# Kernel tuning notes

Measured on AMD Instinct MI355X. Metric: run time of the kernel, lower is better.

Reference implementation:

```python
import jax, jax.numpy as jnp
import numpy as np

N = 100000
E = 1600000
STEPS_IN = 16
IN_DIMS = STEPS_IN + 2  # x concat grid
D = 64  # LATENT_DIMS, mlp_ratio=1 so mid dims == D


def _mlp(x, w1, b1, w2, b2):
    # MLP with mid_dims: Linear -> GELU(exact) -> Linear
    h = jax.nn.gelu(x @ w1 + b1, approximate=False)
    return h @ w2 + b2


def setup_inputs() -> dict:
    key = jax.random.key(0)
    ks = jax.random.split(key, 20)

    def lin(k, fan_in, fan_out):
        bound = 1.0 / np.sqrt(fan_in)
        kw, kb = jax.random.split(k)
        w = jax.random.uniform(kw, (fan_in, fan_out), jnp.float32, -bound, bound)
        b = jax.random.uniform(kb, (fan_out,), jnp.float32, -bound, bound)
        return w, b

    inp = {}
    inp['x'] = jax.random.normal(ks[0], (N, STEPS_IN), jnp.float32)
    inp['grid'] = jax.random.uniform(ks[1], (N, 2), jnp.float32)
    inp['edge_index'] = jax.random.randint(ks[2], (2, E), 0, N, jnp.int64 if jax.config.jax_enable_x64 else jnp.int32)
    inp['edge_features'] = jax.random.normal(ks[3], (E, 5), jnp.float32)

    # project: in_dims -> D (mid D)
    inp['p_w1'], inp['p_b1'] = lin(ks[4], IN_DIMS, D)
    inp['p_w2'], inp['p_b2'] = lin(ks[5], D, D)
    # block W MLP: D -> D (mid D)
    inp['w_w1'], inp['w_b1'] = lin(ks[6], D, D)
    inp['w_w2'], inp['w_b2'] = lin(ks[7], D, D)
    # decode: D -> 1 (mid D)
    inp['d_w1'], inp['d_b1'] = lin(ks[8], D, D)
    inp['d_w2'], inp['d_b2'] = lin(ks[9], D, 1)
    return inp


def reference(x, grid, edge_index, edge_features,
              p_w1, p_b1, p_w2, p_b2,
              w_w1, w_b1, w_w2, w_b2,
              d_w1, d_b1, d_w2, d_b2):
    n = x.shape[0]
    # project node features (x concat grid)
    h = _mlp(jnp.concatenate([x, grid], axis=-1), p_w1, p_b1, p_w2, p_b2)  # [N, D]
    # message passing: message() returns x_j (source features); aggr='add' at target
    src, dst = edge_index[0], edge_index[1]
    msg = h[src]  # [E, D] gather
    aggr = jax.ops.segment_sum(msg, dst, num_segments=n)  # [N, D] scatter-add
    # update (mode 'none'): gelu(W(x) + aggr)
    h = jax.nn.gelu(_mlp(h, w_w1, w_b1, w_w2, w_b2) + aggr, approximate=False)
    # decode to scalar per node
    return _mlp(h, d_w1, d_b1, d_w2, d_b2)  # [N, 1]
```

## Files before the change

### kernel.cpp

```cpp
#include <hip/hip_runtime.h>
#include <math.h>

#define NN 100000
#define NE 1600000
#define D 64
#define INDIM 18
#define CHUNKS 256
#define BN 64
#define NBKT 1563
#define CAP 1536
#define NFRAG 72

typedef __attribute__((ext_vector_type(8))) short s8b;
typedef __attribute__((ext_vector_type(4))) float f32x4;

__device__ __forceinline__ float gelu_exact(float x) {
    return 0.5f * x * (1.0f + erff(x * 0.70710678118654752f));
}

__device__ __forceinline__ void split_bf16(float f, unsigned short& h, unsigned short& l) {
    unsigned int u = __float_as_uint(f);
    unsigned int hb = (u + 0x7FFFu + ((u >> 16) & 1u)) >> 16;
    float hf = __uint_as_float(hb << 16);
    float lo = f - hf;
    unsigned int u2 = __float_as_uint(lo);
    unsigned int lb = (u2 + 0x7FFFu + ((u2 >> 16) & 1u)) >> 16;
    h = (unsigned short)hb; l = (unsigned short)lb;
}

__global__ __launch_bounds__(256) void pack_frags_kernel(
    const float* __restrict__ ww1, const float* __restrict__ ww2,
    const float* __restrict__ dw1, const float* __restrict__ pw1,
    const float* __restrict__ pw2, unsigned short* __restrict__ fragw)
{
    int tid = blockIdx.x * 256 + threadIdx.x;
    if (tid >= NFRAG * 64) return;
    int f = tid >> 6, l = tid & 63;
    unsigned short o[8];
    if (f < 48) {
        int x = f & 1, t = (f >> 1) & 3, s = (f >> 3) & 1, layer = f >> 4;
        const float* W = (layer == 0) ? ww1 : ((layer == 1) ? ww2 : dw1);
        #pragma unroll
        for (int j = 0; j < 8; ++j) {
            int k = s * 32 + (l >> 4) * 8 + j;
            int n = t * 16 + (l & 15);
            unsigned short hh, ll;
            split_bf16(W[k * D + n], hh, ll);
            o[j] = x ? ll : hh;
        }
    } else if (f < 56) {
        int g = f - 48, x = g & 1, t = (g >> 1) & 3;
        #pragma unroll
        for (int j = 0; j < 8; ++j) {
            int k = (l >> 4) * 8 + j;
            int n = t * 16 + (l & 15);
            float v = (k < INDIM) ? pw1[k * D + n] : 0.f;
            unsigned short hh, ll;
            split_bf16(v, hh, ll);
            o[j] = x ? ll : hh;
        }
    } else {
        int g = f - 56, x = g & 1, t = (g >> 1) & 3, s = (g >> 3) & 1;
        #pragma unroll
        for (int j = 0; j < 8; ++j) {
            int k = s * 32 + (l >> 4) * 8 + j;
            int n = t * 16 + (l & 15);
            unsigned short hh, ll;
            split_bf16(pw2[k * D + n], hh, ll);
            o[j] = x ? ll : hh;
        }
    }
    uint4 v;
    v.x = (unsigned)o[0] | ((unsigned)o[1] << 16);
    v.y = (unsigned)o[2] | ((unsigned)o[3] << 16);
    v.z = (unsigned)o[4] | ((unsigned)o[5] << 16);
    v.w = (unsigned)o[6] | ((unsigned)o[7] << 16);
    *(uint4*)&fragw[(size_t)f * 512 + l * 8] = v;
}

__global__ __launch_bounds__(256) void project_mfma(
    const float* __restrict__ x, const float* __restrict__ grid,
    const unsigned short* __restrict__ fragw,
    const float* __restrict__ pb1, const float* __restrict__ pb2,
    float* __restrict__ h)
{
    __shared__ unsigned short midH[64 * 64];
    __shared__ unsigned short midL[64 * 64];
    const int tid = threadIdx.x;
    const int w = tid >> 6, l = tid & 63;
    const int q = l >> 4, c = l & 15;
    const int g0 = blockIdx.x * 64;
    const int rowbase = w * 16;

    union BU { uint4 u; s8b s; };

    const int arow = g0 + rowbase + c;
    const bool ok = arow < NN;
    float fv[8] = {0.f,0.f,0.f,0.f,0.f,0.f,0.f,0.f};
    if (q < 2) {
        if (ok) {
            const float* xp = x + (size_t)arow * 16 + q * 8;
            float4 f0 = *(const float4*)xp;
            float4 f1 = *(const float4*)(xp + 4);
            fv[0]=f0.x; fv[1]=f0.y; fv[2]=f0.z; fv[3]=f0.w;
            fv[4]=f1.x; fv[5]=f1.y; fv[6]=f1.z; fv[7]=f1.w;
        }
    } else if (q == 2) {
        if (ok) {
            float2 g2 = *(const float2*)(grid + (size_t)arow * 2);
            fv[0] = g2.x; fv[1] = g2.y;
        }
    }
    s8b aH[2], aL[2];
    #pragma unroll
    for (int j = 0; j < 8; ++j) {
        unsigned short hh, ll;
        split_bf16(fv[j], hh, ll);
        aH[0][j] = (short)hh; aL[0][j] = (short)ll;
    }

    f32x4 acc[4];
    #pragma unroll
    for (int t = 0; t < 4; ++t) acc[t] = (f32x4){0.f, 0.f, 0.f, 0.f};
    #pragma unroll
    for (int t = 0; t < 4; ++t) {
        BU bh, bl;
        int fb = 48 + t * 2;
        bh.u = *(const uint4*)&fragw[(size_t)fb * 512 + l * 8];
        bl.u = *(const uint4*)&fragw[(size_t)(fb + 1) * 512 + l * 8];
        acc[t] = __builtin_amdgcn_mfma_f32_16x16x32_bf16(aH[0], bh.s, acc[t], 0, 0, 0);
        acc[t] = __builtin_amdgcn_mfma_f32_16x16x32_bf16(aH[0], bl.s, acc[t], 0, 0, 0);
        acc[t] = __builtin_amdgcn_mfma_f32_16x16x32_bf16(aL[0], bh.s, acc[t], 0, 0, 0);
    }

    #pragma unroll
    for (int t = 0; t < 4; ++t) {
        float bias = pb1[t * 16 + c];
        #pragma unroll
        for (int r = 0; r < 4; ++r) {
            int grow = rowbase + q * 4 + r;
            float v = gelu_exact(acc[t][r] + bias);
            unsigned short hh, ll;
            split_bf16(v, hh, ll);
            int byte = ((grow * 128 + (t * 16 + c) * 2)) ^ ((grow & 7) << 4);
            midH[byte >> 1] = hh; midL[byte >> 1] = ll;
        }
    }
    __syncthreads();

    #pragma unroll
    for (int s = 0; s < 2; ++s) {
        int ar = rowbase + c;
        int abyte = (ar * 128 + s * 64 + q * 16) ^ ((ar & 7) << 4);
        aH[s] = *(const s8b*)((const char*)midH + abyte);
        aL[s] = *(const s8b*)((const char*)midL + abyte);
    }
    #pragma unroll
    for (int t = 0; t < 4; ++t) acc[t] = (f32x4){0.f, 0.f, 0.f, 0.f};
    #pragma unroll
    for (int s = 0; s < 2; ++s) {
        #pragma unroll
        for (int t = 0; t < 4; ++t) {
            BU bh, bl;
            int fb = 56 + s * 8 + t * 2;
            bh.u = *(const uint4*)&fragw[(size_t)fb * 512 + l * 8];
            bl.u = *(const uint4*)&fragw[(size_t)(fb + 1) * 512 + l * 8];
            acc[t] = __builtin_amdgcn_mfma_f32_16x16x32_bf16(aH[s], bh.s, acc[t], 0, 0, 0);
            acc[t] = __builtin_amdgcn_mfma_f32_16x16x32_bf16(aH[s], bl.s, acc[t], 0, 0, 0);
            acc[t] = __builtin_amdgcn_mfma_f32_16x16x32_bf16(aL[s], bh.s, acc[t], 0, 0, 0);
        }
    }
    #pragma unroll
    for (int t = 0; t < 4; ++t) {
        float bias = pb2[t * 16 + c];
        #pragma unroll
        for (int r = 0; r < 4; ++r) {
            int row = g0 + rowbase + q * 4 + r;
            if (row < NN) h[(size_t)row * D + t * 16 + c] = acc[t][r] + bias;
        }
    }
}

__global__ __launch_bounds__(256) void project_kernel(
    const float* __restrict__ x, const float* __restrict__ grid,
    const float* __restrict__ w1, const float* __restrict__ b1,
    const float* __restrict__ w2, const float* __restrict__ b2,
    float* __restrict__ h)
{
    int n = blockIdx.x * 256 + threadIdx.x;
    if (n >= NN) return;

    float in[INDIM];
    {
        const float4* xr = (const float4*)(x + (size_t)n * 16);
        float4 a = xr[0], b = xr[1], c = xr[2], d = xr[3];
        in[0]=a.x; in[1]=a.y; in[2]=a.z; in[3]=a.w;
        in[4]=b.x; in[5]=b.y; in[6]=b.z; in[7]=b.w;
        in[8]=c.x; in[9]=c.y; in[10]=c.z; in[11]=c.w;
        in[12]=d.x; in[13]=d.y; in[14]=d.z; in[15]=d.w;
        float2 g = *(const float2*)(grid + (size_t)n * 2);
        in[16]=g.x; in[17]=g.y;
    }

    float mid[D];
    for (int j1 = 0; j1 < D; j1 += 4) {
        float a0 = b1[j1], a1 = b1[j1+1], a2 = b1[j1+2], a3 = b1[j1+3];
        #pragma unroll
        for (int k = 0; k < INDIM; ++k) {
            float t = in[k];
            a0 += t * w1[k*D + j1];
            a1 += t * w1[k*D + j1+1];
            a2 += t * w1[k*D + j1+2];
            a3 += t * w1[k*D + j1+3];
        }
        mid[j1]   = gelu_exact(a0);
        mid[j1+1] = gelu_exact(a1);
        mid[j1+2] = gelu_exact(a2);
        mid[j1+3] = gelu_exact(a3);
    }

    float acc[D];
    #pragma unroll
    for (int j = 0; j < D; ++j) acc[j] = b2[j];
    for (int j1 = 0; j1 < D; j1 += 4) {
        float t0 = mid[j1], t1 = mid[j1+1], t2 = mid[j1+2], t3 = mid[j1+3];
        #pragma unroll
        for (int j = 0; j < D; ++j)
            acc[j] += t0 * w2[j1*D + j]     + t1 * w2[(j1+1)*D + j]
                    + t2 * w2[(j1+2)*D + j] + t3 * w2[(j1+3)*D + j];
    }

    float* hrow = h + (size_t)n * D;
    #pragma unroll
    for (int j = 0; j < D; j += 4) {
        float4 v = { acc[j], acc[j+1], acc[j+2], acc[j+3] };
        *(float4*)(hrow + j) = v;
    }
}

__global__ __launch_bounds__(256) void count_kernel(
    const int* __restrict__ ei, unsigned short* __restrict__ counts)
{
    __shared__ int s_hist[NBKT];
    const int blk = blockIdx.x, tid = threadIdx.x;
    const int* __restrict__ dst = ei + NE;
    for (int i = tid; i < NBKT; i += 256) s_hist[i] = 0;
    __syncthreads();
    for (int e = blk * 256 + tid; e < NE; e += CHUNKS * 256)
        atomicAdd(&s_hist[dst[e] / BN], 1);
    __syncthreads();
    for (int b = tid; b < NBKT; b += 256)
        counts[blk * NBKT + b] = (unsigned short)s_hist[b];
}

__global__ __launch_bounds__(256) void scan_cols_kernel(
    unsigned short* __restrict__ counts, int* __restrict__ btotal)
{
    __shared__ int s[256];
    const int g = blockIdx.x, tid = threadIdx.x;
    int v = counts[tid * NBKT + g];
    s[tid] = v; __syncthreads();
    for (int off = 1; off < 256; off <<= 1) {
        int val = s[tid];
        int add = (tid >= off) ? s[tid - off] : 0;
        __syncthreads();
        s[tid] = val + add;
        __syncthreads();
    }
    counts[tid * NBKT + g] = (unsigned short)(s[tid] - v);
    if (tid == 255) btotal[g] = s[255];
}

__global__ __launch_bounds__(1024) void scan_bsum_kernel(
    const int* __restrict__ btotal, int* __restrict__ offs)
{
    __shared__ int s[1024];
    const int tid = threadIdx.x;
    int b0 = 2 * tid, b1 = 2 * tid + 1;
    int v0 = (b0 < NBKT) ? btotal[b0] : 0;
    int v1 = (b1 < NBKT) ? btotal[b1] : 0;
    int sum = v0 + v1;
    s[tid] = sum; __syncthreads();
    for (int off = 1; off < 1024; off <<= 1) {
        int val = s[tid];
        int add = (tid >= off) ? s[tid - off] : 0;
        __syncthreads();
        s[tid] = val + add;
        __syncthreads();
    }
    int base = s[tid] - sum;
    if (b0 < NBKT) offs[b0] = base;
    if (b1 < NBKT) offs[b1] = base + v0;
    if (tid == 0)  offs[NBKT] = NE;
}

__global__ __launch_bounds__(256) void bin_kernel(
    const int* __restrict__ ei, const unsigned short* __restrict__ counts,
    const int* __restrict__ offs, int* __restrict__ packed)
{
    __shared__ int s_cur[NBKT];
    const int blk = blockIdx.x, tid = threadIdx.x;
    const int* __restrict__ dst = ei + NE;
    for (int b = tid; b < NBKT; b += 256)
        s_cur[b] = offs[b] + (int)counts[blk * NBKT + b];
    __syncthreads();
    for (int e = blk * 256 + tid; e < NE; e += CHUNKS * 256) {
        int d = dst[e];
        int s = ei[e];
        int pos = atomicAdd(&s_cur[d / BN], 1);
        packed[pos] = (s << 6) | (d & (BN - 1));
    }
}

__global__ __launch_bounds__(256) void sortagg_kernel(
    const int* __restrict__ offs, const int* __restrict__ packed,
    const float* __restrict__ h, float* __restrict__ aggr)
{
    __shared__ int s_off[BN + 1];
    __shared__ int s_cur[BN];
    __shared__ int s_src[CAP];
    const int b = blockIdx.x, tid = threadIdx.x;
    const int start = offs[b], end = offs[b + 1];
    const int cnt = end - start;
    const int wid = tid >> 6, lane = tid & 63;
    const int base = b * BN;

    if (cnt <= CAP) {
        if (tid < BN) s_cur[tid] = 0;
        __syncthreads();
        for (int e = start + tid; e < end; e += 256)
            atomicAdd(&s_cur[packed[e] & (BN - 1)], 1);
        __syncthreads();
        if (tid < 64) {
            int v = s_cur[tid];
            int incl = v;
            #pragma unroll
            for (int off = 1; off < 64; off <<= 1) {
                int u = __shfl_up(incl, off, 64);
                if (tid >= off) incl += u;
            }
            s_off[tid] = incl - v;
            if (tid == 63) s_off[64] = cnt;
        }
        __syncthreads();
        if (tid < BN) s_cur[tid] = s_off[tid];
        __syncthreads();
        for (int e = start + tid; e < end; e += 256) {
            int p = packed[e];
            int pos = atomicAdd(&s_cur[p & (BN - 1)], 1);
            s_src[pos] = p >> 6;
        }
        __syncthreads();
        for (int m = wid; m < BN; m += 4) {
            int node = base + m;
            if (node < NN) {
                int s0 = s_off[m], s1 = s_off[m + 1];
                float a0=0,a1=0,a2=0,a3=0,a4=0,a5=0,a6=0,a7=0;
                int e = s0;
                for (; e + 8 <= s1; e += 8) {
                    int i0=s_src[e],  i1=s_src[e+1],i2=s_src[e+2],i3=s_src[e+3];
                    int i4=s_src[e+4],i5=s_src[e+5],i6=s_src[e+6],i7=s_src[e+7];
                    a0 += h[(size_t)i0*D+lane]; a1 += h[(size_t)i1*D+lane];
                    a2 += h[(size_t)i2*D+lane]; a3 += h[(size_t)i3*D+lane];
                    a4 += h[(size_t)i4*D+lane]; a5 += h[(size_t)i5*D+lane];
                    a6 += h[(size_t)i6*D+lane]; a7 += h[(size_t)i7*D+lane];
                }
                for (; e < s1; ++e) a0 += h[(size_t)s_src[e]*D+lane];
                aggr[(size_t)node*D+lane] = ((a0+a1)+(a2+a3))+((a4+a5)+(a6+a7));
            }
        }
    } else {
        for (int m = wid; m < BN; m += 4) {
            int node = base + m;
            if (node < NN) {
                float a = 0.f;
                for (int e = start; e < end; ++e) {
                    int p = packed[e];
                    if ((p & (BN - 1)) == m) a += h[(size_t)(p >> 6) * D + lane];
                }
                aggr[(size_t)node * D + lane] = a;
            }
        }
    }
}

__global__ __launch_bounds__(256) void aggregate_kernel(
    const int* __restrict__ ei, const float* __restrict__ h,
    float* __restrict__ aggr)
{
    int t = blockIdx.x * 256 + threadIdx.x;
    int e = t >> 6;
    int lane = t & 63;
    if (e >= NE) return;
    int src = ei[e];
    int dst = ei[NE + e];
    float v = h[(size_t)src * D + lane];
    atomicAdd(&aggr[(size_t)dst * D + lane], v);
}

__global__ __launch_bounds__(256) void update_decode_mfma(
    const float* __restrict__ h, const float* __restrict__ aggr,
    const unsigned short* __restrict__ fragw,
    const float* __restrict__ wb1, const float* __restrict__ wb2,
    const float* __restrict__ db1, const float* __restrict__ dw2,
    const float* __restrict__ db2, float* __restrict__ out)
{
    __shared__ unsigned short midH[64 * 64];
    __shared__ unsigned short midL[64 * 64];
    const int tid = threadIdx.x;
    const int w = tid >> 6, l = tid & 63;
    const int q = l >> 4, c = l & 15;
    const int g0 = blockIdx.x * 64;
    const int rowbase = w * 16;

    union BU { uint4 u; s8b s; };

    s8b aH[2], aL[2];
    #pragma unroll
    for (int s = 0; s < 2; ++s) {
        const float* hp = h + (size_t)(g0 + rowbase + c) * D + s * 32 + q * 8;
        float4 f0 = *(const float4*)hp;
        float4 f1 = *(const float4*)(hp + 4);
        float fv[8] = {f0.x, f0.y, f0.z, f0.w, f1.x, f1.y, f1.z, f1.w};
        #pragma unroll
        for (int j = 0; j < 8; ++j) {
            unsigned short hh, ll;
            split_bf16(fv[j], hh, ll);
            aH[s][j] = (short)hh; aL[s][j] = (short)ll;
        }
    }

    f32x4 acc[4];
    #pragma unroll
    for (int t = 0; t < 4; ++t) acc[t] = (f32x4){0.f, 0.f, 0.f, 0.f};

    #pragma unroll
    for (int s = 0; s < 2; ++s) {
        #pragma unroll
        for (int t = 0; t < 4; ++t) {
            BU bh, bl;
            int fb = ((0 * 2 + s) * 4 + t) * 2;
            bh.u = *(const uint4*)&fragw[(size_t)fb * 512 + l * 8];
            bl.u = *(const uint4*)&fragw[(size_t)(fb + 1) * 512 + l * 8];
            acc[t] = __builtin_amdgcn_mfma_f32_16x16x32_bf16(aH[s], bh.s, acc[t], 0, 0, 0);
            acc[t] = __builtin_amdgcn_mfma_f32_16x16x32_bf16(aH[s], bl.s, acc[t], 0, 0, 0);
            acc[t] = __builtin_amdgcn_mfma_f32_16x16x32_bf16(aL[s], bh.s, acc[t], 0, 0, 0);
        }
    }

    #pragma unroll
    for (int t = 0; t < 4; ++t) {
        float bias = wb1[t * 16 + c];
        #pragma unroll
        for (int r = 0; r < 4; ++r) {
            int grow = rowbase + q * 4 + r;
            float v = gelu_exact(acc[t][r] + bias);
            unsigned short hh, ll;
            split_bf16(v, hh, ll);
            int byte = ((grow * 128 + (t * 16 + c) * 2)) ^ ((grow & 7) << 4);
            midH[byte >> 1] = hh; midL[byte >> 1] = ll;
        }
    }
    __syncthreads();

    #pragma unroll
    for (int s = 0; s < 2; ++s) {
        int ar = rowbase + c;
        int abyte = (ar * 128 + s * 64 + q * 16) ^ ((ar & 7) << 4);
        aH[s] = *(const s8b*)((const char*)midH + abyte);
        aL[s] = *(const s8b*)((const char*)midL + abyte);
    }
    #pragma unroll
    for (int t = 0; t < 4; ++t) acc[t] = (f32x4){0.f, 0.f, 0.f, 0.f};
    #pragma unroll
    for (int s = 0; s < 2; ++s) {
        #pragma unroll
        for (int t = 0; t < 4; ++t) {
            BU bh, bl;
            int fb = ((1 * 2 + s) * 4 + t) * 2;
            bh.u = *(const uint4*)&fragw[(size_t)fb * 512 + l * 8];
            bl.u = *(const uint4*)&fragw[(size_t)(fb + 1) * 512 + l * 8];
            acc[t] = __builtin_amdgcn_mfma_f32_16x16x32_bf16(aH[s], bh.s, acc[t], 0, 0, 0);
            acc[t] = __builtin_amdgcn_mfma_f32_16x16x32_bf16(aH[s], bl.s, acc[t], 0, 0, 0);
            acc[t] = __builtin_amdgcn_mfma_f32_16x16x32_bf16(aL[s], bh.s, acc[t], 0, 0, 0);
        }
    }
    __syncthreads();

    #pragma unroll
    for (int t = 0; t < 4; ++t) {
        float bias = wb2[t * 16 + c];
        #pragma unroll
        for (int r = 0; r < 4; ++r) {
            int grow = rowbase + q * 4 + r;
            float ag = aggr[(size_t)(g0 + grow) * D + t * 16 + c];
            float v = gelu_exact(acc[t][r] + bias + ag);
            unsigned short hh, ll;
            split_bf16(v, hh, ll);
            int byte = ((grow * 128 + (t * 16 + c) * 2)) ^ ((grow & 7) << 4);
            midH[byte >> 1] = hh; midL[byte >> 1] = ll;
        }
    }
    __syncthreads();

    #pragma unroll
    for (int s = 0; s < 2; ++s) {
        int ar = rowbase + c;
        int abyte = (ar * 128 + s * 64 + q * 16) ^ ((ar & 7) << 4);
        aH[s] = *(const s8b*)((const char*)midH + abyte);
        aL[s] = *(const s8b*)((const char*)midL + abyte);
    }
    #pragma unroll
    for (int t = 0; t < 4; ++t) acc[t] = (f32x4){0.f, 0.f, 0.f, 0.f};
    #pragma unroll
    for (int s = 0; s < 2; ++s) {
        #pragma unroll
        for (int t = 0; t < 4; ++t) {
            BU bh, bl;
            int fb = ((2 * 2 + s) * 4 + t) * 2;
            bh.u = *(const uint4*)&fragw[(size_t)fb * 512 + l * 8];
            bl.u = *(const uint4*)&fragw[(size_t)(fb + 1) * 512 + l * 8];
            acc[t] = __builtin_amdgcn_mfma_f32_16x16x32_bf16(aH[s], bh.s, acc[t], 0, 0, 0);
            acc[t] = __builtin_amdgcn_mfma_f32_16x16x32_bf16(aH[s], bl.s, acc[t], 0, 0, 0);
            acc[t] = __builtin_amdgcn_mfma_f32_16x16x32_bf16(aL[s], bh.s, acc[t], 0, 0, 0);
        }
    }

    float p[4] = {0.f, 0.f, 0.f, 0.f};
    #pragma unroll
    for (int t = 0; t < 4; ++t) {
        float bias = db1[t * 16 + c];
        float wv = dw2[t * 16 + c];
        #pragma unroll
        for (int r = 0; r < 4; ++r)
            p[r] += gelu_exact(acc[t][r] + bias) * wv;
    }
    #pragma unroll
    for (int m = 1; m < 16; m <<= 1) {
        #pragma unroll
        for (int r = 0; r < 4; ++r) p[r] += __shfl_xor(p[r], m, 16);
    }
    if (c == 0) {
        float b2v = db2[0];
        #pragma unroll
        for (int r = 0; r < 4; ++r) {
            int row = g0 + rowbase + q * 4 + r;
            if (row < NN) out[row] = p[r] + b2v;
        }
    }
}

__global__ __launch_bounds__(256) void update_decode_valu(
    const float* __restrict__ h, const float* __restrict__ aggr,
    const float* __restrict__ ww1, const float* __restrict__ wb1,
    const float* __restrict__ ww2, const float* __restrict__ wb2,
    const float* __restrict__ dw1, const float* __restrict__ db1,
    const float* __restrict__ dw2, const float* __restrict__ db2,
    float* __restrict__ out)
{
    int n = blockIdx.x * 256 + threadIdx.x;
    if (n >= NN) return;
    float hrow[D];
    #pragma unroll
    for (int j = 0; j < D; j += 4) {
        float4 v = *(const float4*)(h + (size_t)n * D + j);
        hrow[j] = v.x; hrow[j+1] = v.y; hrow[j+2] = v.z; hrow[j+3] = v.w;
    }
    float mid[D];
    for (int j1 = 0; j1 < D; j1 += 4) {
        float a0 = wb1[j1], a1 = wb1[j1+1], a2 = wb1[j1+2], a3 = wb1[j1+3];
        #pragma unroll
        for (int k = 0; k < D; ++k) {
            float t = hrow[k];
            a0 += t * ww1[k*D + j1];   a1 += t * ww1[k*D + j1+1];
            a2 += t * ww1[k*D + j1+2]; a3 += t * ww1[k*D + j1+3];
        }
        mid[j1]=gelu_exact(a0); mid[j1+1]=gelu_exact(a1);
        mid[j1+2]=gelu_exact(a2); mid[j1+3]=gelu_exact(a3);
    }
    #pragma unroll
    for (int j = 0; j < D; j += 4) {
        float4 v = *(const float4*)(aggr + (size_t)n * D + j);
        hrow[j]=wb2[j]+v.x; hrow[j+1]=wb2[j+1]+v.y;
        hrow[j+2]=wb2[j+2]+v.z; hrow[j+3]=wb2[j+3]+v.w;
    }
    for (int j1 = 0; j1 < D; j1 += 4) {
        float t0=mid[j1], t1=mid[j1+1], t2=mid[j1+2], t3=mid[j1+3];
        #pragma unroll
        for (int j = 0; j < D; ++j)
            hrow[j] += t0*ww2[j1*D+j] + t1*ww2[(j1+1)*D+j]
                     + t2*ww2[(j1+2)*D+j] + t3*ww2[(j1+3)*D+j];
    }
    #pragma unroll
    for (int j = 0; j < D; ++j) hrow[j] = gelu_exact(hrow[j]);
    float o = db2[0];
    for (int j1 = 0; j1 < D; j1 += 4) {
        float a0 = db1[j1], a1 = db1[j1+1], a2 = db1[j1+2], a3 = db1[j1+3];
        #pragma unroll
        for (int k = 0; k < D; ++k) {
            float t = hrow[k];
            a0 += t*dw1[k*D+j1];   a1 += t*dw1[k*D+j1+1];
            a2 += t*dw1[k*D+j1+2]; a3 += t*dw1[k*D+j1+3];
        }
        o += gelu_exact(a0)*dw2[j1] + gelu_exact(a1)*dw2[j1+1]
           + gelu_exact(a2)*dw2[j1+2] + gelu_exact(a3)*dw2[j1+3];
    }
    out[n] = o;
}

extern "C" void kernel_launch(void* const* d_in, const int* in_sizes, int n_in,
                              void* d_out, int out_size, void* d_ws, size_t ws_size,
                              hipStream_t stream) {
    const float* x    = (const float*)d_in[0];
    const float* grid = (const float*)d_in[1];
    const int*   ei   = (const int*)d_in[2];
    const float* p_w1 = (const float*)d_in[4];
    const float* p_b1 = (const float*)d_in[5];
    const float* p_w2 = (const float*)d_in[6];
    const float* p_b2 = (const float*)d_in[7];
    const float* w_w1 = (const float*)d_in[8];
    const float* w_b1 = (const float*)d_in[9];
    const float* w_w2 = (const float*)d_in[10];
    const float* w_b2 = (const float*)d_in[11];
    const float* d_w1 = (const float*)d_in[12];
    const float* d_b1 = (const float*)d_in[13];
    const float* d_w2 = (const float*)d_in[14];
    const float* d_b2 = (const float*)d_in[15];
    float* out = (float*)d_out;

    float* h    = (float*)d_ws;
    float* aggr = h + (size_t)NN * D;
    unsigned short* counts = (unsigned short*)(aggr + (size_t)NN * D);
    int* btotal = (int*)(counts + (size_t)CHUNKS * NBKT);
    int* offs   = btotal + NBKT;
    int* packed = offs + NBKT + 1;
    unsigned short* fragw =
        (unsigned short*)((((uintptr_t)(packed + NE)) + 15) & ~(uintptr_t)15);

    size_t need = ((char*)(fragw + NFRAG * 512)) - (char*)d_ws;

    if (ws_size >= need) {
        pack_frags_kernel<<<(NFRAG * 64 + 255) / 256, 256, 0, stream>>>(
            w_w1, w_w2, d_w1, p_w1, p_w2, fragw);
        project_mfma<<<(NN + 63) / 64, 256, 0, stream>>>(
            x, grid, fragw, p_b1, p_b2, h);
        count_kernel    <<<CHUNKS, 256, 0, stream>>>(ei, counts);
        scan_cols_kernel<<<NBKT,   256, 0, stream>>>(counts, btotal);
        scan_bsum_kernel<<<1,     1024, 0, stream>>>(btotal, offs);
        bin_kernel      <<<CHUNKS, 256, 0, stream>>>(ei, counts, offs, packed);
        sortagg_kernel  <<<NBKT,   256, 0, stream>>>(offs, packed, h, aggr);
        update_decode_mfma<<<(NN + 63) / 64, 256, 0, stream>>>(
            h, aggr, fragw, w_b1, w_b2, d_b1, d_w2, d_b2, out);
    } else {
        project_kernel<<<(NN + 255) / 256, 256, 0, stream>>>(
            x, grid, p_w1, p_b1, p_w2, p_b2, h);
        hipMemsetAsync(aggr, 0, (size_t)NN * D * sizeof(float), stream);
        aggregate_kernel<<<(size_t)NE * 64 / 256, 256, 0, stream>>>(ei, h, aggr);
        update_decode_valu<<<(NN + 255) / 256, 256, 0, stream>>>(
            h, aggr, w_w1, w_b1, w_w2, w_b2, d_w1, d_b1, d_w2, d_b2, out);
    }
}
```

Baseline: 160.1 us.

## Fuse sorted aggregation with update/decode MLP and widen binning chunk count

Merges the per-bucket gather-sum kernel with the update and decode MFMA kernel, keeping the aggregated features in shared memory instead of writing and rereading a global aggr array, and drops one launch. Separately raises CHUNKS from 256 to 1024 so the count and bin kernels run more blocks, with the column scan now handling four counts per thread. The fused kernel uses more shared memory (an extra 64x65 float tile), which can reduce occupancy during the latency-bound gather. The workspace still reserves space sized by CHUNKS, so the size check must accommodate the larger counts array, or the code falls back to the slower path.

```diff
diff --git a/kernel.cpp b/kernel.cpp
--- a/kernel.cpp
+++ b/kernel.cpp
@@ -5,7 +5,7 @@
 #define NE 1600000
 #define D 64
 #define INDIM 18
-#define CHUNKS 256
+#define CHUNKS 1024
 #define BN 64
 #define NBKT 1563
 #define CAP 1536
@@ -250,7 +250,7 @@
         atomicAdd(&s_hist[dst[e] / BN], 1);
     __syncthreads();
     for (int b = tid; b < NBKT; b += 256)
-        counts[blk * NBKT + b] = (unsigned short)s_hist[b];
+        counts[(size_t)blk * NBKT + b] = (unsigned short)s_hist[b];
 }
 
 __global__ __launch_bounds__(256) void scan_cols_kernel(
@@ -258,8 +258,12 @@
 {
     __shared__ int s[256];
     const int g = blockIdx.x, tid = threadIdx.x;
-    int v = counts[tid * NBKT + g];
-    s[tid] = v; __syncthreads();
+    int c[4];
+    #pragma unroll
+    for (int i = 0; i < 4; ++i)
+        c[i] = counts[(size_t)(tid * 4 + i) * NBKT + g];
+    int sum = c[0] + c[1] + c[2] + c[3];
+    s[tid] = sum; __syncthreads();
     for (int off = 1; off < 256; off <<= 1) {
         int val = s[tid];
         int add = (tid >= off) ? s[tid - off] : 0;
@@ -267,7 +271,12 @@
         s[tid] = val + add;
         __syncthreads();
     }
-    counts[tid * NBKT + g] = (unsigned short)(s[tid] - v);
+    int base = s[tid] - sum;
+    #pragma unroll
+    for (int i = 0; i < 4; ++i) {
+        counts[(size_t)(tid * 4 + i) * NBKT + g] = (unsigned short)base;
+        base += c[i];
+    }
     if (tid == 255) btotal[g] = s[255];
 }
 
@@ -302,7 +311,7 @@
     const int blk = blockIdx.x, tid = threadIdx.x;
     const int* __restrict__ dst = ei + NE;
     for (int b = tid; b < NBKT; b += 256)
-        s_cur[b] = offs[b] + (int)counts[blk * NBKT + b];
+        s_cur[b] = offs[b] + (int)counts[(size_t)blk * NBKT + b];
     __syncthreads();
     for (int e = blk * 256 + tid; e < NE; e += CHUNKS * 256) {
         int d = dst[e];
@@ -312,13 +321,19 @@
     }
 }
 
-__global__ __launch_bounds__(256) void sortagg_kernel(
+__global__ __launch_bounds__(256) void sortagg_update_kernel(
     const int* __restrict__ offs, const int* __restrict__ packed,
-    const float* __restrict__ h, float* __restrict__ aggr)
+    const float* __restrict__ h, const unsigned short* __restrict__ fragw,
+    const float* __restrict__ wb1, const float* __restrict__ wb2,
+    const float* __restrict__ db1, const float* __restrict__ dw2,
+    const float* __restrict__ db2, float* __restrict__ out)
 {
     __shared__ int s_off[BN + 1];
     __shared__ int s_cur[BN];
     __shared__ int s_src[CAP];
+    __shared__ float s_aggr[BN][65];
+    __shared__ unsigned short midH[64 * 64];
+    __shared__ unsigned short midL[64 * 64];
     const int b = blockIdx.x, tid = threadIdx.x;
     const int start = offs[b], end = offs[b + 1];
     const int cnt = end - start;
@@ -352,34 +367,169 @@
         }
         __syncthreads();
         for (int m = wid; m < BN; m += 4) {
-            int node = base + m;
-            if (node < NN) {
-                int s0 = s_off[m], s1 = s_off[m + 1];
-                float a0=0,a1=0,a2=0,a3=0,a4=0,a5=0,a6=0,a7=0;
-                int e = s0;
-                for (; e + 8 <= s1; e += 8) {
-                    int i0=s_src[e],  i1=s_src[e+1],i2=s_src[e+2],i3=s_src[e+3];
-                    int i4=s_src[e+4],i5=s_src[e+5],i6=s_src[e+6],i7=s_src[e+7];
-                    a0 += h[(size_t)i0*D+lane]; a1 += h[(size_t)i1*D+lane];
-                    a2 += h[(size_t)i2*D+lane]; a3 += h[(size_t)i3*D+lane];
-                    a4 += h[(size_t)i4*D+lane]; a5 += h[(size_t)i5*D+lane];
-                    a6 += h[(size_t)i6*D+lane]; a7 += h[(size_t)i7*D+lane];
-                }
-                for (; e < s1; ++e) a0 += h[(size_t)s_src[e]*D+lane];
-                aggr[(size_t)node*D+lane] = ((a0+a1)+(a2+a3))+((a4+a5)+(a6+a7));
+            int s0 = s_off[m], s1 = s_off[m + 1];
+            float a0=0,a1=0,a2=0,a3=0,a4=0,a5=0,a6=0,a7=0;
+            int e = s0;
+            for (; e + 8 <= s1; e += 8) {
+                int i0=s_src[e],  i1=s_src[e+1],i2=s_src[e+2],i3=s_src[e+3];
+                int i4=s_src[e+4],i5=s_src[e+5],i6=s_src[e+6],i7=s_src[e+7];
+                a0 += h[(size_t)i0*D+lane]; a1 += h[(size_t)i1*D+lane];
+                a2 += h[(size_t)i2*D+lane]; a3 += h[(size_t)i3*D+lane];
+                a4 += h[(size_t)i4*D+lane]; a5 += h[(size_t)i5*D+lane];
+                a6 += h[(size_t)i6*D+lane]; a7 += h[(size_t)i7*D+lane];
             }
+            for (; e < s1; ++e) a0 += h[(size_t)s_src[e]*D+lane];
+            s_aggr[m][lane] = ((a0+a1)+(a2+a3))+((a4+a5)+(a6+a7));
         }
     } else {
         for (int m = wid; m < BN; m += 4) {
-            int node = base + m;
-            if (node < NN) {
-                float a = 0.f;
-                for (int e = start; e < end; ++e) {
-                    int p = packed[e];
-                    if ((p & (BN - 1)) == m) a += h[(size_t)(p >> 6) * D + lane];
-                }
-                aggr[(size_t)node * D + lane] = a;
+            float a = 0.f;
+            for (int e = start; e < end; ++e) {
+                int p = packed[e];
+                if ((p & (BN - 1)) == m) a += h[(size_t)(p >> 6) * D + lane];
             }
+            s_aggr[m][lane] = a;
+        }
+    }
+    __syncthreads();
+
+    const int w = wid, l = lane;
+    const int q = l >> 4, c = l & 15;
+    const int g0 = base;
+    const int rowbase = w * 16;
+
+    union BU { uint4 u; s8b s; };
+
+    s8b aH[2], aL[2];
+    #pragma unroll
+    for (int s = 0; s < 2; ++s) {
+        const float* hp = h + (size_t)(g0 + rowbase + c) * D + s * 32 + q * 8;
+        float4 f0 = *(const float4*)hp;
+        float4 f1 = *(const float4*)(hp + 4);
+        float fv[8] = {f0.x, f0.y, f0.z, f0.w, f1.x, f1.y, f1.z, f1.w};
+        #pragma unroll
+        for (int j = 0; j < 8; ++j) {
+            unsigned short hh, ll;
+            split_bf16(fv[j], hh, ll);
+            aH[s][j] = (short)hh; aL[s][j] = (short)ll;
+        }
+    }
+
+    f32x4 acc[4];
+    #pragma unroll
+    for (int t = 0; t < 4; ++t) acc[t] = (f32x4){0.f, 0.f, 0.f, 0.f};
+    #pragma unroll
+    for (int s = 0; s < 2; ++s) {
+        #pragma unroll
+        for (int t = 0; t < 4; ++t) {
+            BU bh, bl;
+            int fb = ((0 * 2 + s) * 4 + t) * 2;
+            bh.u = *(const uint4*)&fragw[(size_t)fb * 512 + l * 8];
+            bl.u = *(const uint4*)&fragw[(size_t)(fb + 1) * 512 + l * 8];
+            acc[t] = __builtin_amdgcn_mfma_f32_16x16x32_bf16(aH[s], bh.s, acc[t], 0, 0, 0);
+            acc[t] = __builtin_amdgcn_mfma_f32_16x16x32_bf16(aH[s], bl.s, acc[t], 0, 0, 0);
+            acc[t] = __builtin_amdgcn_mfma_f32_16x16x32_bf16(aL[s], bh.s, acc[t], 0, 0, 0);
+        }
+    }
+
+    #pragma unroll
+    for (int t = 0; t < 4; ++t) {
+        float bias = wb1[t * 16 + c];
+        #pragma unroll
+        for (int r = 0; r < 4; ++r) {
+            int grow = rowbase + q * 4 + r;
+            float v = gelu_exact(acc[t][r] + bias);
+            unsigned short hh, ll;
+            split_bf16(v, hh, ll);
+            int byte = ((grow * 128 + (t * 16 + c) * 2)) ^ ((grow & 7) << 4);
+            midH[byte >> 1] = hh; midL[byte >> 1] = ll;
+        }
+    }
+    __syncthreads();
+
+    #pragma unroll
+    for (int s = 0; s < 2; ++s) {
+        int ar = rowbase + c;
+        int abyte = (ar * 128 + s * 64 + q * 16) ^ ((ar & 7) << 4);
+        aH[s] = *(const s8b*)((const char*)midH + abyte);
+        aL[s] = *(const s8b*)((const char*)midL + abyte);
+    }
+    #pragma unroll
+    for (int t = 0; t < 4; ++t) acc[t] = (f32x4){0.f, 0.f, 0.f, 0.f};
+    #pragma unroll
+    for (int s = 0; s < 2; ++s) {
+        #pragma unroll
+        for (int t = 0; t < 4; ++t) {
+            BU bh, bl;
+            int fb = ((1 * 2 + s) * 4 + t) * 2;
+            bh.u = *(const uint4*)&fragw[(size_t)fb * 512 + l * 8];
+            bl.u = *(const uint4*)&fragw[(size_t)(fb + 1) * 512 + l * 8];
+            acc[t] = __builtin_amdgcn_mfma_f32_16x16x32_bf16(aH[s], bh.s, acc[t], 0, 0, 0);
+            acc[t] = __builtin_amdgcn_mfma_f32_16x16x32_bf16(aH[s], bl.s, acc[t], 0, 0, 0);
+            acc[t] = __builtin_amdgcn_mfma_f32_16x16x32_bf16(aL[s], bh.s, acc[t], 0, 0, 0);
+        }
+    }
+    __syncthreads();
+
+    #pragma unroll
+    for (int t = 0; t < 4; ++t) {
+        float bias = wb2[t * 16 + c];
+        #pragma unroll
+        for (int r = 0; r < 4; ++r) {
+            int grow = rowbase + q * 4 + r;
+            float ag = s_aggr[grow][t * 16 + c];
+            float v = gelu_exact(acc[t][r] + bias + ag);
+            unsigned short hh, ll;
+            split_bf16(v, hh, ll);
+            int byte = ((grow * 128 + (t * 16 + c) * 2)) ^ ((grow & 7) << 4);
+            midH[byte >> 1] = hh; midL[byte >> 1] = ll;
+        }
+    }
+    __syncthreads();
+
+    #pragma unroll
+    for (int s = 0; s < 2; ++s) {
+        int ar = rowbase + c;
+        int abyte = (ar * 128 + s * 64 + q * 16) ^ ((ar & 7) << 4);
+        aH[s] = *(const s8b*)((const char*)midH + abyte);
+        aL[s] = *(const s8b*)((const char*)midL + abyte);
+    }
+    #pragma unroll
+    for (int t = 0; t < 4; ++t) acc[t] = (f32x4){0.f, 0.f, 0.f, 0.f};
+    #pragma unroll
+    for (int s = 0; s < 2; ++s) {
+        #pragma unroll
+        for (int t = 0; t < 4; ++t) {
+            BU bh, bl;
+            int fb = ((2 * 2 + s) * 4 + t) * 2;
+            bh.u = *(const uint4*)&fragw[(size_t)fb * 512 + l * 8];
+            bl.u = *(const uint4*)&fragw[(size_t)(fb + 1) * 512 + l * 8];
+            acc[t] = __builtin_amdgcn_mfma_f32_16x16x32_bf16(aH[s], bh.s, acc[t], 0, 0, 0);
+            acc[t] = __builtin_amdgcn_mfma_f32_16x16x32_bf16(aH[s], bl.s, acc[t], 0, 0, 0);
+            acc[t] = __builtin_amdgcn_mfma_f32_16x16x32_bf16(aL[s], bh.s, acc[t], 0, 0, 0);
+        }
+    }
+
+    float p[4] = {0.f, 0.f, 0.f, 0.f};
+    #pragma unroll
+    for (int t = 0; t < 4; ++t) {
+        float bias = db1[t * 16 + c];
+        float wv = dw2[t * 16 + c];
+        #pragma unroll
+        for (int r = 0; r < 4; ++r)
+            p[r] += gelu_exact(acc[t][r] + bias) * wv;
+    }
+    #pragma unroll
+    for (int m = 1; m < 16; m <<= 1) {
+        #pragma unroll
+        for (int r = 0; r < 4; ++r) p[r] += __shfl_xor(p[r], m, 16);
+    }
+    if (c == 0) {
+        float b2v = db2[0];
+        #pragma unroll
+        for (int r = 0; r < 4; ++r) {
+            int row = g0 + rowbase + q * 4 + r;
+            if (row < NN) out[row] = p[r] + b2v;
         }
     }
 }
@@ -396,158 +546,6 @@
     int dst = ei[NE + e];
     float v = h[(size_t)src * D + lane];
     atomicAdd(&aggr[(size_t)dst * D + lane], v);
-}
-
-__global__ __launch_bounds__(256) void update_decode_mfma(
-    const float* __restrict__ h, const float* __restrict__ aggr,
-    const unsigned short* __restrict__ fragw,
-    const float* __restrict__ wb1, const float* __restrict__ wb2,
-    const float* __restrict__ db1, const float* __restrict__ dw2,
-    const float* __restrict__ db2, float* __restrict__ out)
-{
-    __shared__ unsigned short midH[64 * 64];
-    __shared__ unsigned short midL[64 * 64];
-    const int tid = threadIdx.x;
-    const int w = tid >> 6, l = tid & 63;
-    const int q = l >> 4, c = l & 15;
-    const int g0 = blockIdx.x * 64;
-    const int rowbase = w * 16;
-
-    union BU { uint4 u; s8b s; };
-
-    s8b aH[2], aL[2];
-    #pragma unroll
-    for (int s = 0; s < 2; ++s) {
-        const float* hp = h + (size_t)(g0 + rowbase + c) * D + s * 32 + q * 8;
-        float4 f0 = *(const float4*)hp;
-        float4 f1 = *(const float4*)(hp + 4);
-        float fv[8] = {f0.x, f0.y, f0.z, f0.w, f1.x, f1.y, f1.z, f1.w};
-        #pragma unroll
-        for (int j = 0; j < 8; ++j) {
-            unsigned short hh, ll;
-            split_bf16(fv[j], hh, ll);
-            aH[s][j] = (short)hh; aL[s][j] = (short)ll;
-        }
-    }
-
-    f32x4 acc[4];
-    #pragma unroll
-    for (int t = 0; t < 4; ++t) acc[t] = (f32x4){0.f, 0.f, 0.f, 0.f};
-
-    #pragma unroll
-    for (int s = 0; s < 2; ++s) {
-        #pragma unroll
-        for (int t = 0; t < 4; ++t) {
-            BU bh, bl;
-            int fb = ((0 * 2 + s) * 4 + t) * 2;
-            bh.u = *(const uint4*)&fragw[(size_t)fb * 512 + l * 8];
-            bl.u = *(const uint4*)&fragw[(size_t)(fb + 1) * 512 + l * 8];
-            acc[t] = __builtin_amdgcn_mfma_f32_16x16x32_bf16(aH[s], bh.s, acc[t], 0, 0, 0);
-            acc[t] = __builtin_amdgcn_mfma_f32_16x16x32_bf16(aH[s], bl.s, acc[t], 0, 0, 0);
-            acc[t] = __builtin_amdgcn_mfma_f32_16x16x32_bf16(aL[s], bh.s, acc[t], 0, 0, 0);
-        }
-    }
-
-    #pragma unroll
-    for (int t = 0; t < 4; ++t) {
-        float bias = wb1[t * 16 + c];
-        #pragma unroll
-        for (int r = 0; r < 4; ++r) {
-            int grow = rowbase + q * 4 + r;
-            float v = gelu_exact(acc[t][r] + bias);
-            unsigned short hh, ll;
-            split_bf16(v, hh, ll);
-            int byte = ((grow * 128 + (t * 16 + c) * 2)) ^ ((grow & 7) << 4);
-            midH[byte >> 1] = hh; midL[byte >> 1] = ll;
-        }
-    }
-    __syncthreads();
-
-    #pragma unroll
-    for (int s = 0; s < 2; ++s) {
-        int ar = rowbase + c;
-        int abyte = (ar * 128 + s * 64 + q * 16) ^ ((ar & 7) << 4);
-        aH[s] = *(const s8b*)((const char*)midH + abyte);
-        aL[s] = *(const s8b*)((const char*)midL + abyte);
-    }
-    #pragma unroll
-    for (int t = 0; t < 4; ++t) acc[t] = (f32x4){0.f, 0.f, 0.f, 0.f};
-    #pragma unroll
-    for (int s = 0; s < 2; ++s) {
-        #pragma unroll
-        for (int t = 0; t < 4; ++t) {
-            BU bh, bl;
-            int fb = ((1 * 2 + s) * 4 + t) * 2;
-            bh.u = *(const uint4*)&fragw[(size_t)fb * 512 + l * 8];
-            bl.u = *(const uint4*)&fragw[(size_t)(fb + 1) * 512 + l * 8];
-            acc[t] = __builtin_amdgcn_mfma_f32_16x16x32_bf16(aH[s], bh.s, acc[t], 0, 0, 0);
-            acc[t] = __builtin_amdgcn_mfma_f32_16x16x32_bf16(aH[s], bl.s, acc[t], 0, 0, 0);
-            acc[t] = __builtin_amdgcn_mfma_f32_16x16x32_bf16(aL[s], bh.s, acc[t], 0, 0, 0);
-        }
-    }
-    __syncthreads();
-
-    #pragma unroll
-    for (int t = 0; t < 4; ++t) {
-        float bias = wb2[t * 16 + c];
-        #pragma unroll
-        for (int r = 0; r < 4; ++r) {
-            int grow = rowbase + q * 4 + r;
-            float ag = aggr[(size_t)(g0 + grow) * D + t * 16 + c];
-            float v = gelu_exact(acc[t][r] + bias + ag);
-            unsigned short hh, ll;
-            split_bf16(v, hh, ll);
-            int byte = ((grow * 128 + (t * 16 + c) * 2)) ^ ((grow & 7) << 4);
-            midH[byte >> 1] = hh; midL[byte >> 1] = ll;
-        }
-    }
-    __syncthreads();
-
-    #pragma unroll
-    for (int s = 0; s < 2; ++s) {
-        int ar = rowbase + c;
-        int abyte = (ar * 128 + s * 64 + q * 16) ^ ((ar & 7) << 4);
-        aH[s] = *(const s8b*)((const char*)midH + abyte);
-        aL[s] = *(const s8b*)((const char*)midL + abyte);
-    }
-    #pragma unroll
-    for (int t = 0; t < 4; ++t) acc[t] = (f32x4){0.f, 0.f, 0.f, 0.f};
-    #pragma unroll
-    for (int s = 0; s < 2; ++s) {
-        #pragma unroll
-        for (int t = 0; t < 4; ++t) {
-            BU bh, bl;
-            int fb = ((2 * 2 + s) * 4 + t) * 2;
-            bh.u = *(const uint4*)&fragw[(size_t)fb * 512 + l * 8];
-            bl.u = *(const uint4*)&fragw[(size_t)(fb + 1) * 512 + l * 8];
-            acc[t] = __builtin_amdgcn_mfma_f32_16x16x32_bf16(aH[s], bh.s, acc[t], 0, 0, 0);
-            acc[t] = __builtin_amdgcn_mfma_f32_16x16x32_bf16(aH[s], bl.s, acc[t], 0, 0, 0);
-            acc[t] = __builtin_amdgcn_mfma_f32_16x16x32_bf16(aL[s], bh.s, acc[t], 0, 0, 0);
-        }
-    }
-
-    float p[4] = {0.f, 0.f, 0.f, 0.f};
-    #pragma unroll
-    for (int t = 0; t < 4; ++t) {
-        float bias = db1[t * 16 + c];
-        float wv = dw2[t * 16 + c];
-        #pragma unroll
-        for (int r = 0; r < 4; ++r)
-            p[r] += gelu_exact(acc[t][r] + bias) * wv;
-    }
-    #pragma unroll
-    for (int m = 1; m < 16; m <<= 1) {
-        #pragma unroll
-        for (int r = 0; r < 4; ++r) p[r] += __shfl_xor(p[r], m, 16);
-    }
-    if (c == 0) {
-        float b2v = db2[0];
-        #pragma unroll
-        for (int r = 0; r < 4; ++r) {
-            int row = g0 + rowbase + q * 4 + r;
-            if (row < NN) out[row] = p[r] + b2v;
-        }
-    }
 }
 
 __global__ __launch_bounds__(256) void update_decode_valu(
@@ -648,9 +646,8 @@
         scan_cols_kernel<<<NBKT,   256, 0, stream>>>(counts, btotal);
         scan_bsum_kernel<<<1,     1024, 0, stream>>>(btotal, offs);
         bin_kernel      <<<CHUNKS, 256, 0, stream>>>(ei, counts, offs, packed);
-        sortagg_kernel  <<<NBKT,   256, 0, stream>>>(offs, packed, h, aggr);
-        update_decode_mfma<<<(NN + 63) / 64, 256, 0, stream>>>(
-            h, aggr, fragw, w_b1, w_b2, d_b1, d_w2, d_b2, out);
+        sortagg_update_kernel<<<NBKT, 256, 0, stream>>>(
+            offs, packed, h, fragw, w_b1, w_b2, d_b1, d_w2, d_b2, out);
     } else {
         project_kernel<<<(NN + 255) / 256, 256, 0, stream>>>(
             x, grid, p_w1, p_b1, p_w2, p_b2, h);
```

New measurement: 184.5 us. +15.3%, slower.

## Replace per-chunk count matrix and column scan with global atomics and bucket reservation

Applied to the files above, without the earlier changes.

The counting sort for edge binning no longer writes a 256×1563 per-chunk count matrix and scans its columns. Each chunk now adds its bucket histogram into a global degree array with atomics, a single scan produces offsets and cursors, and the bin kernel recomputes its local histogram and reserves ranges with global atomicAdd on the cursors. This drops one kernel launch and the count-matrix traffic, at the cost of reading dst twice in the bin kernel and adding global atomic contention. It also adds a memset. The order of edges within a bucket becomes nondeterministic across chunks, which could change floating-point summation order.

```diff
diff --git a/kernel.cpp b/kernel.cpp
--- a/kernel.cpp
+++ b/kernel.cpp
@@ -5,7 +5,7 @@
 #define NE 1600000
 #define D 64
 #define INDIM 18
-#define CHUNKS 256
+#define NCHK 256
 #define BN 64
 #define NBKT 1563
 #define CAP 1536
@@ -239,46 +239,30 @@
 }
 
 __global__ __launch_bounds__(256) void count_kernel(
-    const int* __restrict__ ei, unsigned short* __restrict__ counts)
+    const int* __restrict__ ei, int* __restrict__ deg)
 {
     __shared__ int s_hist[NBKT];
     const int blk = blockIdx.x, tid = threadIdx.x;
     const int* __restrict__ dst = ei + NE;
     for (int i = tid; i < NBKT; i += 256) s_hist[i] = 0;
     __syncthreads();
-    for (int e = blk * 256 + tid; e < NE; e += CHUNKS * 256)
+    for (int e = blk * 256 + tid; e < NE; e += NCHK * 256)
         atomicAdd(&s_hist[dst[e] / BN], 1);
     __syncthreads();
-    for (int b = tid; b < NBKT; b += 256)
-        counts[blk * NBKT + b] = (unsigned short)s_hist[b];
-}
-
-__global__ __launch_bounds__(256) void scan_cols_kernel(
-    unsigned short* __restrict__ counts, int* __restrict__ btotal)
-{
-    __shared__ int s[256];
-    const int g = blockIdx.x, tid = threadIdx.x;
-    int v = counts[tid * NBKT + g];
-    s[tid] = v; __syncthreads();
-    for (int off = 1; off < 256; off <<= 1) {
-        int val = s[tid];
-        int add = (tid >= off) ? s[tid - off] : 0;
-        __syncthreads();
-        s[tid] = val + add;
-        __syncthreads();
-    }
-    counts[tid * NBKT + g] = (unsigned short)(s[tid] - v);
-    if (tid == 255) btotal[g] = s[255];
+    for (int b = tid; b < NBKT; b += 256) {
+        int c = s_hist[b];
+        if (c) atomicAdd(&deg[b], c);
+    }
 }
 
 __global__ __launch_bounds__(1024) void scan_bsum_kernel(
-    const int* __restrict__ btotal, int* __restrict__ offs)
+    const int* __restrict__ deg, int* __restrict__ offs, int* __restrict__ cursor)
 {
     __shared__ int s[1024];
     const int tid = threadIdx.x;
     int b0 = 2 * tid, b1 = 2 * tid + 1;
-    int v0 = (b0 < NBKT) ? btotal[b0] : 0;
-    int v1 = (b1 < NBKT) ? btotal[b1] : 0;
+    int v0 = (b0 < NBKT) ? deg[b0] : 0;
+    int v1 = (b1 < NBKT) ? deg[b1] : 0;
     int sum = v0 + v1;
     s[tid] = sum; __syncthreads();
     for (int off = 1; off < 1024; off <<= 1) {
@@ -289,22 +273,29 @@
         __syncthreads();
     }
     int base = s[tid] - sum;
-    if (b0 < NBKT) offs[b0] = base;
-    if (b1 < NBKT) offs[b1] = base + v0;
+    if (b0 < NBKT) { offs[b0] = base;      cursor[b0] = base; }
+    if (b1 < NBKT) { offs[b1] = base + v0; cursor[b1] = base + v0; }
     if (tid == 0)  offs[NBKT] = NE;
 }
 
-__global__ __launch_bounds__(256) void bin_kernel(
-    const int* __restrict__ ei, const unsigned short* __restrict__ counts,
-    const int* __restrict__ offs, int* __restrict__ packed)
+__global__ __launch_bounds__(256) void bin_reserve_kernel(
+    const int* __restrict__ ei, int* __restrict__ cursor,
+    int* __restrict__ packed)
 {
     __shared__ int s_cur[NBKT];
     const int blk = blockIdx.x, tid = threadIdx.x;
     const int* __restrict__ dst = ei + NE;
-    for (int b = tid; b < NBKT; b += 256)
-        s_cur[b] = offs[b] + (int)counts[blk * NBKT + b];
-    __syncthreads();
-    for (int e = blk * 256 + tid; e < NE; e += CHUNKS * 256) {
+    for (int i = tid; i < NBKT; i += 256) s_cur[i] = 0;
+    __syncthreads();
+    for (int e = blk * 256 + tid; e < NE; e += NCHK * 256)
+        atomicAdd(&s_cur[dst[e] / BN], 1);
+    __syncthreads();
+    for (int b = tid; b < NBKT; b += 256) {
+        int c = s_cur[b];
+        s_cur[b] = c ? atomicAdd(&cursor[b], c) : 0;
+    }
+    __syncthreads();
+    for (int e = blk * 256 + tid; e < NE; e += NCHK * 256) {
         int d = dst[e];
         int s = ei[e];
         int pos = atomicAdd(&s_cur[d / BN], 1);
@@ -630,10 +621,10 @@
 
     float* h    = (float*)d_ws;
     float* aggr = h + (size_t)NN * D;
-    unsigned short* counts = (unsigned short*)(aggr + (size_t)NN * D);
-    int* btotal = (int*)(counts + (size_t)CHUNKS * NBKT);
-    int* offs   = btotal + NBKT;
-    int* packed = offs + NBKT + 1;
+    int* deg    = (int*)(aggr + (size_t)NN * D);
+    int* offs   = deg + NBKT;
+    int* cursor = offs + NBKT + 1;
+    int* packed = cursor + NBKT;
     unsigned short* fragw =
         (unsigned short*)((((uintptr_t)(packed + NE)) + 15) & ~(uintptr_t)15);
 
@@ -642,13 +633,13 @@
     if (ws_size >= need) {
         pack_frags_kernel<<<(NFRAG * 64 + 255) / 256, 256, 0, stream>>>(
             w_w1, w_w2, d_w1, p_w1, p_w2, fragw);
+        hipMemsetAsync(deg, 0, NBKT * sizeof(int), stream);
         project_mfma<<<(NN + 63) / 64, 256, 0, stream>>>(
             x, grid, fragw, p_b1, p_b2, h);
-        count_kernel    <<<CHUNKS, 256, 0, stream>>>(ei, counts);
-        scan_cols_kernel<<<NBKT,   256, 0, stream>>>(counts, btotal);
-        scan_bsum_kernel<<<1,     1024, 0, stream>>>(btotal, offs);
-        bin_kernel      <<<CHUNKS, 256, 0, stream>>>(ei, counts, offs, packed);
-        sortagg_kernel  <<<NBKT,   256, 0, stream>>>(offs, packed, h, aggr);
+        count_kernel      <<<NCHK, 256, 0, stream>>>(ei, deg);
+        scan_bsum_kernel  <<<1,   1024, 0, stream>>>(deg, offs, cursor);
+        bin_reserve_kernel<<<NCHK, 256, 0, stream>>>(ei, cursor, packed);
+        sortagg_kernel    <<<NBKT, 256, 0, stream>>>(offs, packed, h, aggr);
         update_decode_mfma<<<(NN + 63) / 64, 256, 0, stream>>>(
             h, aggr, fragw, w_b1, w_b2, d_b1, d_w2, d_b2, out);
     } else {
```

After: 170.5 us. 1.07x slower.
